# Optimization experiments

Hardware: AMD Instinct MI355X
Metric: run time of the kernel (lower is better)

## Reference

```python
import jax, jax.numpy as jnp
import numpy as np

NPOINT = 1024
RADIUS = 0.2
NSAMPLE = 32
FILTERS = [64, 64, 128]
BN_EPS = 1e-3  # Keras BatchNormalization default epsilon


def setup_inputs() -> dict:
    key = jax.random.key(0)
    ks = jax.random.split(key, 2 + 4 * len(FILTERS))
    xyz = jax.random.uniform(ks[0], (8, 4096, 3), dtype=jnp.float32)
    points = jax.random.normal(ks[1], (8, 4096, 64), dtype=jnp.float32)
    inp = {"xyz": xyz, "points": points}
    c_in = 64 + 3  # use_xyz concat
    for i, f in enumerate(FILTERS):
        k = 2 + 4 * i
        inp[f"w{i}"] = jax.random.normal(ks[k], (c_in, f), dtype=jnp.float32) * (1.0 / np.sqrt(c_in))
        inp[f"b{i}"] = jnp.zeros((f,), jnp.float32)
        inp[f"g{i}"] = 1.0 + 0.1 * jax.random.normal(ks[k + 2], (f,), dtype=jnp.float32)
        inp[f"be{i}"] = 0.1 * jax.random.normal(ks[k + 3], (f,), dtype=jnp.float32)
        c_in = f
    return inp


def farthest_point_sample(npoint, xyz):
    # xyz: (B, A, 3) -> idx (B, npoint), sequential FPS starting at point 0
    B, A, _ = xyz.shape
    def step(carry, _):
        dists, farthest = carry
        centroid = jnp.take_along_axis(xyz, farthest[:, None, None], axis=1)  # (B,1,3)
        d = jnp.sum((xyz - centroid) ** 2, axis=-1)                            # (B,A)
        dists = jnp.minimum(dists, d)
        nxt = jnp.argmax(dists, axis=-1).astype(jnp.int32)
        return (dists, nxt), farthest
    init = (jnp.full((B, A), 1e10, xyz.dtype), jnp.zeros((B,), jnp.int32))
    _, idx = jax.lax.scan(step, init, None, length=npoint)  # (npoint, B)
    return idx.T  # (B, npoint)


def query_ball_point(radius, nsample, xyz, new_xyz):
    # xyz: (B,A,3), new_xyz: (B,N,3) -> idx (B,N,nsample)
    A = xyz.shape[1]
    d2 = jnp.sum((new_xyz[:, :, None, :] - xyz[:, None, :, :]) ** 2, axis=-1)  # (B,N,A)
    mask = d2 < radius * radius
    cand = jnp.where(mask, jnp.arange(A, dtype=jnp.int32), jnp.int32(A))
    cand = jnp.sort(cand, axis=-1)[..., :nsample]           # first in-ball indices
    first = cand[..., :1]
    idx = jnp.where(cand == A, first, cand)                  # pad with first found
    idx = jnp.where(idx == A, 0, idx)                        # empty ball -> 0
    return idx


def group_point(points, idx):
    # points: (B,A,C), idx: (B,N,S) -> (B,N,S,C)
    return jax.vmap(lambda p, i: p[i])(points, idx)


def _forward(xyz, points, params):
    fps_idx = jax.lax.stop_gradient(farthest_point_sample(NPOINT, xyz))
    new_xyz = jnp.take_along_axis(xyz, fps_idx[:, :, None], axis=1)          # (B,N,3)
    idx = query_ball_point(RADIUS, NSAMPLE, jax.lax.stop_gradient(xyz),
                           jax.lax.stop_gradient(new_xyz))
    grouped_xyz = group_point(xyz, idx) - new_xyz[:, :, None, :]             # (B,N,S,3)
    grouped = jnp.concatenate([group_point(points, idx), grouped_xyz], -1)   # (B,N,S,C+3)
    h = grouped
    for (w, b, g, be) in params:
        h = jnp.einsum('bnsc,cf->bnsf', h, w) + b    # shared 1x1 conv
        h = g * h / jnp.sqrt(1.0 + BN_EPS) + be      # inference BN (mean=0, var=1)
        h = jax.nn.relu(h)
    new_points = jnp.max(h, axis=2)                  # max-pool over nsample
    return new_xyz, new_points


def reference(xyz, points, w0, b0, g0, be0, w1, b1, g1, be1, w2, b2, g2, be2):
    params = [(w0, b0, g0, be0), (w1, b1, g1, be1), (w2, b2, g2, be2)]
    return _forward(xyz, points, params)
```

## Files before the change

kernel.cpp:

```cpp
#include <hip/hip_runtime.h>

#define NPTS 4096
#define NQ   1024
#define NB   8
#define XTW  36

#define FPS_T  512
#define FPS_W  8
#define PPT    8
#define FPS_NB 8
#define WRK_NB 240
#define NWRK   (WRK_NB * 8)
#define WSLICE 10496
#define SMEM_BYTES (WSLICE * 8)

template <int CTRL, int RM>
__device__ __forceinline__ int dppi(int v) {
  return __builtin_amdgcn_update_dpp(v, v, CTRL, RM, 0xf, false);
}

template <int CTRL, int RM>
__device__ __forceinline__ double dpp_keymax(double k) {
  long long i = __double_as_longlong(k);
  int lo = (int)(unsigned)((unsigned long long)i & 0xffffffffull);
  int hi = (int)(unsigned)((unsigned long long)i >> 32);
  int plo = dppi<CTRL, RM>(lo);
  int phi = dppi<CTRL, RM>(hi);
  double o = __longlong_as_double(
      (long long)(((unsigned long long)(unsigned)phi << 32) | (unsigned)plo));
  return fmax(k, o);
}

__device__ __forceinline__ double wave_keymax(double k) {
  k = dpp_keymax<0x111, 0xf>(k);
  k = dpp_keymax<0x112, 0xf>(k);
  k = dpp_keymax<0x114, 0xf>(k);
  k = dpp_keymax<0x118, 0xf>(k);
  k = dpp_keymax<0x142, 0xa>(k);
  k = dpp_keymax<0x143, 0xc>(k);
  return k;
}

template <int C>
__device__ __forceinline__ float dppq(float v) {
  return __int_as_float(__builtin_amdgcn_update_dpp(
      __float_as_int(v), __float_as_int(v), C, 0xf, 0xf, false));
}

__device__ void fps_role(const float* __restrict__ xyz,
                         float* __restrict__ out_newxyz,
                         int* __restrict__ ws_idx, char* smem)
{
  const int b    = blockIdx.x;
  const int t    = threadIdx.x;
  const int lane = t & 63;
  const int wave = t >> 6;

  float* sxyz4 = (float*)smem;
  double (*swk)[FPS_W] = (double(*)[FPS_W])(smem + NPTS * 16);

  const float* xb = xyz + (size_t)b * NPTS * 3;
  for (int p = t; p < NPTS; p += FPS_T) {
    sxyz4[p * 4 + 0] = xb[p * 3 + 0];
    sxyz4[p * 4 + 1] = xb[p * 3 + 1];
    sxyz4[p * 4 + 2] = xb[p * 3 + 2];
    sxyz4[p * 4 + 3] = 0.0f;
  }
  __syncthreads();

  float px[PPT], py[PPT], pz[PPT], dst[PPT];
  unsigned ilo[PPT];
#pragma unroll
  for (int k = 0; k < PPT; ++k) {
    int p = t + (k << 9);
    px[k] = sxyz4[p * 4 + 0];
    py[k] = sxyz4[p * 4 + 1];
    pz[k] = sxyz4[p * 4 + 2];
    dst[k] = 1e10f;
    ilo[k] = ~(unsigned)p;
  }

  int farh0 = 0, farh1 = 0;
  int far = 0;
  for (int n = 0; n < NQ; ++n) {
    const float4 c = *(const float4*)(sxyz4 + far * 4);
    if (t == 0)
      __hip_atomic_store(ws_idx + (b << 10) + n, far,
                         __ATOMIC_RELAXED, __HIP_MEMORY_SCOPE_AGENT);
    if ((n & (FPS_T - 1)) == t) {
      if (n >> 9) farh1 = far; else farh0 = far;
    }

    double kk[PPT];
#pragma unroll
    for (int k = 0; k < PPT; ++k) {
      float dx = __fsub_rn(px[k], c.x);
      float dy = __fsub_rn(py[k], c.y);
      float dz = __fsub_rn(pz[k], c.z);
      float d2 = __fadd_rn(__fadd_rn(__fmul_rn(dx, dx), __fmul_rn(dy, dy)),
                           __fmul_rn(dz, dz));
      float dm = fminf(dst[k], d2);
      dst[k] = dm;
      kk[k] = __longlong_as_double((long long)(
          ((unsigned long long)__float_as_uint(dm) << 32) | ilo[k]));
    }
    double m0 = fmax(kk[0], kk[1]);
    double m1 = fmax(kk[2], kk[3]);
    double m2 = fmax(kk[4], kk[5]);
    double m3 = fmax(kk[6], kk[7]);
    double best = fmax(fmax(m0, m1), fmax(m2, m3));
    best = wave_keymax(best);

    long long bi = __double_as_longlong(best);
    unsigned blo = (unsigned)__builtin_amdgcn_readlane(
        (int)(unsigned)((unsigned long long)bi & 0xffffffffull), 63);
    unsigned bhi = (unsigned)__builtin_amdgcn_readlane(
        (int)(unsigned)((unsigned long long)bi >> 32), 63);
    double wkey = __longlong_as_double(
        (long long)(((unsigned long long)bhi << 32) | blo));

    const int par = n & 1;
    if (lane == 0) swk[par][wave] = wkey;
    __syncthreads();

    const double2* sp = (const double2*)swk[par];
    double2 a0 = sp[0], a1 = sp[1], a2 = sp[2], a3 = sp[3];
    double mk = fmax(fmax(fmax(a0.x, a0.y), fmax(a1.x, a1.y)),
                     fmax(fmax(a2.x, a2.y), fmax(a3.x, a3.y)));
    far = (int)(~(unsigned)((unsigned long long)__double_as_longlong(mk)));
  }

  {
    float4 c0 = *(const float4*)(sxyz4 + farh0 * 4);
    float* o0 = out_newxyz + ((size_t)b * NQ + t) * 3;
    o0[0] = c0.x; o0[1] = c0.y; o0[2] = c0.z;
    float4 c1 = *(const float4*)(sxyz4 + farh1 * 4);
    float* o1 = out_newxyz + ((size_t)b * NQ + FPS_T + t) * 3;
    o1[0] = c1.x; o1[1] = c1.y; o1[2] = c1.z;
  }
}

__device__ __forceinline__ void mlp_acc(float* __restrict__ acc,
                                        const float* __restrict__ XTb,
                                        const float* __restrict__ wg,
                                        int ldw, int nk, int fg, int sg)
{
#pragma unroll
  for (int i = 0; i < 32; ++i) acc[i] = 0.0f;
  const float* xrow = XTb + sg * 4;
  const float* wrow = wg + fg * 8;
#pragma unroll 4
  for (int k = 0; k < nk; ++k) {
    const float4 x  = *(const float4*)(xrow + k * XTW);
    const float4 wa = *(const float4*)(wrow + (size_t)k * ldw);
    const float4 wb = *(const float4*)(wrow + (size_t)k * ldw + 4);
    acc[0]  = fmaf(wa.x, x.x, acc[0]);  acc[1]  = fmaf(wa.x, x.y, acc[1]);
    acc[2]  = fmaf(wa.x, x.z, acc[2]);  acc[3]  = fmaf(wa.x, x.w, acc[3]);
    acc[4]  = fmaf(wa.y, x.x, acc[4]);  acc[5]  = fmaf(wa.y, x.y, acc[5]);
    acc[6]  = fmaf(wa.y, x.z, acc[6]);  acc[7]  = fmaf(wa.y, x.w, acc[7]);
    acc[8]  = fmaf(wa.z, x.x, acc[8]);  acc[9]  = fmaf(wa.z, x.y, acc[9]);
    acc[10] = fmaf(wa.z, x.z, acc[10]); acc[11] = fmaf(wa.z, x.w, acc[11]);
    acc[12] = fmaf(wa.w, x.x, acc[12]); acc[13] = fmaf(wa.w, x.y, acc[13]);
    acc[14] = fmaf(wa.w, x.z, acc[14]); acc[15] = fmaf(wa.w, x.w, acc[15]);
    acc[16] = fmaf(wb.x, x.x, acc[16]); acc[17] = fmaf(wb.x, x.y, acc[17]);
    acc[18] = fmaf(wb.x, x.z, acc[18]); acc[19] = fmaf(wb.x, x.w, acc[19]);
    acc[20] = fmaf(wb.y, x.x, acc[20]); acc[21] = fmaf(wb.y, x.y, acc[21]);
    acc[22] = fmaf(wb.y, x.z, acc[22]); acc[23] = fmaf(wb.y, x.w, acc[23]);
    acc[24] = fmaf(wb.z, x.x, acc[24]); acc[25] = fmaf(wb.z, x.y, acc[25]);
    acc[26] = fmaf(wb.z, x.z, acc[26]); acc[27] = fmaf(wb.z, x.w, acc[27]);
    acc[28] = fmaf(wb.w, x.x, acc[28]); acc[29] = fmaf(wb.w, x.y, acc[29]);
    acc[30] = fmaf(wb.w, x.z, acc[30]); acc[31] = fmaf(wb.w, x.w, acc[31]);
  }
}

__device__ __forceinline__ void store_layer(const float* __restrict__ acc,
                                            float* __restrict__ XTb,
                                            const float* __restrict__ g,
                                            const float* __restrict__ bi,
                                            const float* __restrict__ be,
                                            int fg, int sg, float RSQ)
{
  const float4 ga = *(const float4*)(g  + fg * 8);
  const float4 gb = *(const float4*)(g  + fg * 8 + 4);
  const float4 ba = *(const float4*)(bi + fg * 8);
  const float4 bb = *(const float4*)(bi + fg * 8 + 4);
  const float4 ea = *(const float4*)(be + fg * 8);
  const float4 eb = *(const float4*)(be + fg * 8 + 4);
  float sv[8] = {ga.x * RSQ, ga.y * RSQ, ga.z * RSQ, ga.w * RSQ,
                 gb.x * RSQ, gb.y * RSQ, gb.z * RSQ, gb.w * RSQ};
  float bv[8] = {ba.x, ba.y, ba.z, ba.w, bb.x, bb.y, bb.z, bb.w};
  float ev[8] = {ea.x, ea.y, ea.z, ea.w, eb.x, eb.y, eb.z, eb.w};
#pragma unroll
  for (int j = 0; j < 8; ++j) {
    float tv = fmaf(bv[j], sv[j], ev[j]);
    float4 h;
    h.x = fmaxf(fmaf(acc[j * 4 + 0], sv[j], tv), 0.0f);
    h.y = fmaxf(fmaf(acc[j * 4 + 1], sv[j], tv), 0.0f);
    h.z = fmaxf(fmaf(acc[j * 4 + 2], sv[j], tv), 0.0f);
    h.w = fmaxf(fmaf(acc[j * 4 + 3], sv[j], tv), 0.0f);
    *(float4*)(XTb + (fg * 8 + j) * XTW + sg * 4) = h;
  }
}

__device__ void worker_query(int q, int idx,
    const float* __restrict__ xyz, const float* __restrict__ pts,
    const float* __restrict__ w0, const float* __restrict__ b0,
    const float* __restrict__ g0, const float* __restrict__ be0,
    const float* __restrict__ w1, const float* __restrict__ b1,
    const float* __restrict__ g1, const float* __restrict__ be1,
    const float* __restrict__ w2, const float* __restrict__ b2,
    const float* __restrict__ g2, const float* __restrict__ be2,
    float* __restrict__ outp, float* __restrict__ XT, int* __restrict__ bidx,
    int lane)
{
  const int b = q >> 10;
  const float* xb = xyz + (size_t)b * NPTS * 3;
  const float cx = xb[idx * 3 + 0];
  const float cy = xb[idx * 3 + 1];
  const float cz = xb[idx * 3 + 2];

  int cnt = 0;
  float x0 = xb[lane * 3 + 0], y0 = xb[lane * 3 + 1], z0 = xb[lane * 3 + 2];
  float x1 = xb[(64 + lane) * 3 + 0], y1 = xb[(64 + lane) * 3 + 1],
        z1 = xb[(64 + lane) * 3 + 2];
  for (int ch = 0; ch < 64; ++ch) {
    const int an = (min(ch + 2, 63) << 6) | lane;
    float nx = xb[an * 3 + 0], ny = xb[an * 3 + 1], nz = xb[an * 3 + 2];
    float dx = __fsub_rn(cx, x0);
    float dy = __fsub_rn(cy, y0);
    float dz = __fsub_rn(cz, z0);
    float d2 = __fadd_rn(__fadd_rn(__fmul_rn(dx, dx), __fmul_rn(dy, dy)),
                         __fmul_rn(dz, dz));
    bool in = d2 < 0.04f;
    unsigned long long bal = __ballot(in);
    int pos = cnt + (int)__popcll(bal & ((1ull << lane) - 1ull));
    if (in && pos < 32) bidx[pos] = (ch << 6) | lane;
    cnt += (int)__popcll(bal);
    x0 = x1; y0 = y1; z0 = z1;
    x1 = nx; y1 = ny; z1 = nz;
    if (cnt >= 32) break;
  }
  if (cnt > 32) cnt = 32;
  int i0 = bidx[0];
  if (lane < 32 && lane >= cnt) bidx[lane] = i0;
  __builtin_amdgcn_wave_barrier();

  const int s  = lane & 31;
  const int kc = lane >> 5;
  const int is = bidx[s];
  const float4* pr4 = (const float4*)(pts + ((size_t)(b * NPTS + is)) * 64 + kc * 32);
  float* xcol = XT + s;
#pragma unroll
  for (int c = 0; c < 8; ++c) {
    float4 v = pr4[c];
    xcol[(kc * 32 + c * 4 + 0) * XTW] = v.x;
    xcol[(kc * 32 + c * 4 + 1) * XTW] = v.y;
    xcol[(kc * 32 + c * 4 + 2) * XTW] = v.z;
    xcol[(kc * 32 + c * 4 + 3) * XTW] = v.w;
  }
  if (kc == 0) {
    float ax = xb[is * 3 + 0], ay = xb[is * 3 + 1], az = xb[is * 3 + 2];
    xcol[64 * XTW] = ax - cx;
    xcol[65 * XTW] = ay - cy;
    xcol[66 * XTW] = az - cz;
  }
  __builtin_amdgcn_wave_barrier();

  const int fg = lane >> 3;
  const int sg = lane & 7;
  const float RSQ = rsqrtf(1.0f + 0.001f);
  float acc[32];

  mlp_acc(acc, XT, w0, 64, 67, fg, sg);
  store_layer(acc, XT, g0, b0, be0, fg, sg, RSQ);
  __builtin_amdgcn_wave_barrier();

  mlp_acc(acc, XT, w1, 64, 64, fg, sg);
  store_layer(acc, XT, g1, b1, be1, fg, sg, RSQ);
  __builtin_amdgcn_wave_barrier();

#pragma unroll
  for (int pass = 0; pass < 2; ++pass) {
    const int fofs = pass << 6;
    mlp_acc(acc, XT, w2 + fofs, 128, 64, fg, sg);
    const float4 ga = *(const float4*)(g2  + fofs + fg * 8);
    const float4 gb = *(const float4*)(g2  + fofs + fg * 8 + 4);
    const float4 ba = *(const float4*)(b2  + fofs + fg * 8);
    const float4 bb = *(const float4*)(b2  + fofs + fg * 8 + 4);
    const float4 ea = *(const float4*)(be2 + fofs + fg * 8);
    const float4 eb = *(const float4*)(be2 + fofs + fg * 8 + 4);
    float sv[8] = {ga.x * RSQ, ga.y * RSQ, ga.z * RSQ, ga.w * RSQ,
                   gb.x * RSQ, gb.y * RSQ, gb.z * RSQ, gb.w * RSQ};
    float bv[8] = {ba.x, ba.y, ba.z, ba.w, bb.x, bb.y, bb.z, bb.w};
    float ev[8] = {ea.x, ea.y, ea.z, ea.w, eb.x, eb.y, eb.z, eb.w};
    float r[8];
#pragma unroll
    for (int j = 0; j < 8; ++j) {
      float mx = fmaxf(fmaxf(acc[j * 4 + 0], acc[j * 4 + 1]),
                       fmaxf(acc[j * 4 + 2], acc[j * 4 + 3]));
      float mn = fminf(fminf(acc[j * 4 + 0], acc[j * 4 + 1]),
                       fminf(acc[j * 4 + 2], acc[j * 4 + 3]));
      mx = fmaxf(mx, dppq<0xB1>(mx));
      mx = fmaxf(mx, dppq<0x4E>(mx));
      mx = fmaxf(mx, dppq<0x141>(mx));
      mn = fminf(mn, dppq<0xB1>(mn));
      mn = fminf(mn, dppq<0x4E>(mn));
      mn = fminf(mn, dppq<0x141>(mn));
      float tv = fmaf(bv[j], sv[j], ev[j]);
      float m  = (sv[j] >= 0.0f) ? mx : mn;
      r[j] = fmaxf(fmaf(sv[j], m, tv), 0.0f);
    }
    if (sg == 0) {
      float* o = outp + (size_t)q * 128 + fofs + fg * 8;
      *(float4*)(o)     = make_float4(r[0], r[1], r[2], r[3]);
      *(float4*)(o + 4) = make_float4(r[4], r[5], r[6], r[7]);
    }
  }
}

__global__ __launch_bounds__(FPS_T, 1) void fused_kernel(
    const float* __restrict__ xyz, const float* __restrict__ pts,
    const float* __restrict__ w0, const float* __restrict__ b0,
    const float* __restrict__ g0, const float* __restrict__ be0,
    const float* __restrict__ w1, const float* __restrict__ b1,
    const float* __restrict__ g1, const float* __restrict__ be1,
    const float* __restrict__ w2, const float* __restrict__ b2,
    const float* __restrict__ g2, const float* __restrict__ be2,
    float* __restrict__ newxyz, float* __restrict__ newpts,
    int* __restrict__ ws_idx)
{
  __shared__ __align__(16) char smem[SMEM_BYTES];

  if (blockIdx.x < FPS_NB) {
    fps_role(xyz, newxyz, ws_idx, smem);
    return;
  }

  const int lane = threadIdx.x & 63;
  const int wave = threadIdx.x >> 6;
  char* sl = smem + wave * WSLICE;
  float* XT  = (float*)sl;
  int* bidx  = (int*)(sl + 9648);

  const int W = (blockIdx.x - FPS_NB) * 8 + wave;
  for (int g = W; g < NB * NQ; g += NWRK) {
    const int b = g & 7;
    const int n = g >> 3;
    const int q = (b << 10) | n;

    const int* slot = ws_idx + q;
    int idx = __hip_atomic_load(slot, __ATOMIC_RELAXED, __HIP_MEMORY_SCOPE_AGENT);
    int spins = 0;
    while ((unsigned)idx >= (unsigned)NPTS) {
      __builtin_amdgcn_s_sleep(16);
      idx = __hip_atomic_load(slot, __ATOMIC_RELAXED, __HIP_MEMORY_SCOPE_AGENT);
      if (++spins > 32768) { idx &= (NPTS - 1); break; }
    }

    worker_query(q, idx, xyz, pts, w0, b0, g0, be0, w1, b1, g1, be1,
                 w2, b2, g2, be2, newpts, XT, bidx, lane);
  }
}

extern "C" void kernel_launch(void* const* d_in, const int* in_sizes, int n_in,
                              void* d_out, int out_size, void* d_ws, size_t ws_size,
                              hipStream_t stream)
{
  const float* xyz = (const float*)d_in[0];
  const float* pts = (const float*)d_in[1];
  const float* w0  = (const float*)d_in[2];
  const float* b0  = (const float*)d_in[3];
  const float* g0  = (const float*)d_in[4];
  const float* be0 = (const float*)d_in[5];
  const float* w1  = (const float*)d_in[6];
  const float* b1  = (const float*)d_in[7];
  const float* g1  = (const float*)d_in[8];
  const float* be1 = (const float*)d_in[9];
  const float* w2  = (const float*)d_in[10];
  const float* b2  = (const float*)d_in[11];
  const float* g2  = (const float*)d_in[12];
  const float* be2 = (const float*)d_in[13];

  float* out    = (float*)d_out;
  float* newxyz = out;
  float* newpts = out + NB * NQ * 3;
  int*   ws_idx = (int*)d_ws;

  hipMemsetAsync(d_ws, 0xAA, (size_t)NB * NQ * sizeof(int), stream);

  hipLaunchKernelGGL(fused_kernel, dim3(FPS_NB + WRK_NB), dim3(FPS_T), 0, stream,
                     xyz, pts, w0, b0, g0, be0, w1, b1, g1, be1,
                     w2, b2, g2, be2, newxyz, newpts, ws_idx);
}
```

Measured before the change: 666.6 us.

## Restructure FPS to four waves with float max and ballot argmax

The farthest-point-sampling role now uses only 4 of its 8 waves, each thread holding 16 points, so the per-iteration block reduction combines fewer partials. The packed 64-bit key max reduction is replaced by a float max reduction across the wave, followed by a ballot pass to recover the lowest matching index. Sampled indices are also batched and published 8 at a time instead of one store per iteration. The aim is to shorten the serial per-iteration latency of FPS, at the cost of more work per thread and extra ballot instructions.

```diff
diff --git a/kernel.cpp b/kernel.cpp
--- a/kernel.cpp
+++ b/kernel.cpp
@@ -6,8 +6,8 @@
 #define XTW  36
 
 #define FPS_T  512
-#define FPS_W  8
-#define PPT    8
+#define FPW    4
+#define SLOTS  16
 #define FPS_NB 8
 #define WRK_NB 240
 #define NWRK   (WRK_NB * 8)
@@ -15,30 +15,19 @@
 #define SMEM_BYTES (WSLICE * 8)
 
 template <int CTRL, int RM>
-__device__ __forceinline__ int dppi(int v) {
-  return __builtin_amdgcn_update_dpp(v, v, CTRL, RM, 0xf, false);
-}
-
-template <int CTRL, int RM>
-__device__ __forceinline__ double dpp_keymax(double k) {
-  long long i = __double_as_longlong(k);
-  int lo = (int)(unsigned)((unsigned long long)i & 0xffffffffull);
-  int hi = (int)(unsigned)((unsigned long long)i >> 32);
-  int plo = dppi<CTRL, RM>(lo);
-  int phi = dppi<CTRL, RM>(hi);
-  double o = __longlong_as_double(
-      (long long)(((unsigned long long)(unsigned)phi << 32) | (unsigned)plo));
-  return fmax(k, o);
-}
-
-__device__ __forceinline__ double wave_keymax(double k) {
-  k = dpp_keymax<0x111, 0xf>(k);
-  k = dpp_keymax<0x112, 0xf>(k);
-  k = dpp_keymax<0x114, 0xf>(k);
-  k = dpp_keymax<0x118, 0xf>(k);
-  k = dpp_keymax<0x142, 0xa>(k);
-  k = dpp_keymax<0x143, 0xc>(k);
-  return k;
+__device__ __forceinline__ float dppf(float v) {
+  return __int_as_float(__builtin_amdgcn_update_dpp(
+      __float_as_int(v), __float_as_int(v), CTRL, RM, 0xf, false));
+}
+
+__device__ __forceinline__ float wave_max_f(float v) {
+  v = fmaxf(v, dppf<0x111, 0xf>(v));
+  v = fmaxf(v, dppf<0x112, 0xf>(v));
+  v = fmaxf(v, dppf<0x114, 0xf>(v));
+  v = fmaxf(v, dppf<0x118, 0xf>(v));
+  v = fmaxf(v, dppf<0x142, 0xa>(v));
+  v = fmaxf(v, dppf<0x143, 0xc>(v));
+  return v;
 }
 
 template <int C>
@@ -57,7 +46,7 @@
   const int wave = t >> 6;
 
   float* sxyz4 = (float*)smem;
-  double (*swk)[FPS_W] = (double(*)[FPS_W])(smem + NPTS * 16);
+  double (*swk)[FPW] = (double(*)[FPW])(smem + NPTS * 16);
 
   const float* xb = xyz + (size_t)b * NPTS * 3;
   for (int p = t; p < NPTS; p += FPS_T) {
@@ -68,75 +57,81 @@
   }
   __syncthreads();
 
-  float px[PPT], py[PPT], pz[PPT], dst[PPT];
-  unsigned ilo[PPT];
-#pragma unroll
-  for (int k = 0; k < PPT; ++k) {
-    int p = t + (k << 9);
-    px[k] = sxyz4[p * 4 + 0];
-    py[k] = sxyz4[p * 4 + 1];
-    pz[k] = sxyz4[p * 4 + 2];
-    dst[k] = 1e10f;
-    ilo[k] = ~(unsigned)p;
-  }
-
-  int farh0 = 0, farh1 = 0;
+  float px[SLOTS], py[SLOTS], pz[SLOTS], dst[SLOTS];
+  if (wave < FPW) {
+#pragma unroll
+    for (int k = 0; k < SLOTS; ++k) {
+      int p = t + (k << 8);
+      px[k] = sxyz4[p * 4 + 0];
+      py[k] = sxyz4[p * 4 + 1];
+      pz[k] = sxyz4[p * 4 + 2];
+      dst[k] = 1e10f;
+    }
+  }
+
   int far = 0;
+  int fkeep = 0;
+  int farh[4] = {0, 0, 0, 0};
+
   for (int n = 0; n < NQ; ++n) {
-    const float4 c = *(const float4*)(sxyz4 + far * 4);
-    if (t == 0)
-      __hip_atomic_store(ws_idx + (b << 10) + n, far,
-                         __ATOMIC_RELAXED, __HIP_MEMORY_SCOPE_AGENT);
-    if ((n & (FPS_T - 1)) == t) {
-      if (n >> 9) farh1 = far; else farh0 = far;
-    }
-
-    double kk[PPT];
-#pragma unroll
-    for (int k = 0; k < PPT; ++k) {
-      float dx = __fsub_rn(px[k], c.x);
-      float dy = __fsub_rn(py[k], c.y);
-      float dz = __fsub_rn(pz[k], c.z);
-      float d2 = __fadd_rn(__fadd_rn(__fmul_rn(dx, dx), __fmul_rn(dy, dy)),
-                           __fmul_rn(dz, dz));
-      float dm = fminf(dst[k], d2);
-      dst[k] = dm;
-      kk[k] = __longlong_as_double((long long)(
-          ((unsigned long long)__float_as_uint(dm) << 32) | ilo[k]));
-    }
-    double m0 = fmax(kk[0], kk[1]);
-    double m1 = fmax(kk[2], kk[3]);
-    double m2 = fmax(kk[4], kk[5]);
-    double m3 = fmax(kk[6], kk[7]);
-    double best = fmax(fmax(m0, m1), fmax(m2, m3));
-    best = wave_keymax(best);
-
-    long long bi = __double_as_longlong(best);
-    unsigned blo = (unsigned)__builtin_amdgcn_readlane(
-        (int)(unsigned)((unsigned long long)bi & 0xffffffffull), 63);
-    unsigned bhi = (unsigned)__builtin_amdgcn_readlane(
-        (int)(unsigned)((unsigned long long)bi >> 32), 63);
-    double wkey = __longlong_as_double(
-        (long long)(((unsigned long long)bhi << 32) | blo));
-
-    const int par = n & 1;
-    if (lane == 0) swk[par][wave] = wkey;
+    if (wave < FPW) {
+      const float4 c = *(const float4*)(sxyz4 + far * 4);
+      if (wave == 0 && lane == (n & 7)) fkeep = far;
+      if ((n & 255) == t) farh[n >> 8] = far;
+
+#pragma unroll
+      for (int k = 0; k < SLOTS; ++k) {
+        float dx = __fsub_rn(px[k], c.x);
+        float dy = __fsub_rn(py[k], c.y);
+        float dz = __fsub_rn(pz[k], c.z);
+        float d2 = __fadd_rn(__fadd_rn(__fmul_rn(dx, dx), __fmul_rn(dy, dy)),
+                             __fmul_rn(dz, dz));
+        dst[k] = fminf(dst[k], d2);
+      }
+      float m0 = fmaxf(fmaxf(dst[0],  dst[1]),  dst[2]);
+      float m1 = fmaxf(fmaxf(dst[3],  dst[4]),  dst[5]);
+      float m2 = fmaxf(fmaxf(dst[6],  dst[7]),  dst[8]);
+      float m3 = fmaxf(fmaxf(dst[9],  dst[10]), dst[11]);
+      float m4 = fmaxf(fmaxf(dst[12], dst[13]), dst[14]);
+      float ma = fmaxf(fmaxf(m0, m1), m2);
+      float mb = fmaxf(fmaxf(m3, m4), dst[15]);
+      float m  = fmaxf(ma, mb);
+      m = wave_max_f(m);
+      const float ms = __int_as_float(
+          __builtin_amdgcn_readlane(__float_as_int(m), 63));
+
+      int idxw = 0;
+#pragma unroll
+      for (int k = SLOTS - 1; k >= 0; --k) {
+        unsigned long long mask = __ballot(dst[k] == ms);
+        if (mask) idxw = (k << 8) + (wave << 6) + (int)__builtin_ctzll(mask);
+      }
+      if (lane == 0) {
+        unsigned long long kb =
+            ((unsigned long long)__float_as_uint(ms) << 32) |
+            (unsigned)(~(unsigned)idxw);
+        swk[n & 1][wave] = __longlong_as_double((long long)kb);
+      }
+    }
     __syncthreads();
-
-    const double2* sp = (const double2*)swk[par];
-    double2 a0 = sp[0], a1 = sp[1], a2 = sp[2], a3 = sp[3];
-    double mk = fmax(fmax(fmax(a0.x, a0.y), fmax(a1.x, a1.y)),
-                     fmax(fmax(a2.x, a2.y), fmax(a3.x, a3.y)));
-    far = (int)(~(unsigned)((unsigned long long)__double_as_longlong(mk)));
-  }
-
-  {
-    float4 c0 = *(const float4*)(sxyz4 + farh0 * 4);
-    float* o0 = out_newxyz + ((size_t)b * NQ + t) * 3;
-    o0[0] = c0.x; o0[1] = c0.y; o0[2] = c0.z;
-    float4 c1 = *(const float4*)(sxyz4 + farh1 * 4);
-    float* o1 = out_newxyz + ((size_t)b * NQ + FPS_T + t) * 3;
-    o1[0] = c1.x; o1[1] = c1.y; o1[2] = c1.z;
+    if (wave < FPW) {
+      const double2* sp = (const double2*)swk[n & 1];
+      double2 a0 = sp[0], a1 = sp[1];
+      double mk = fmax(fmax(a0.x, a0.y), fmax(a1.x, a1.y));
+      far = (int)(~(unsigned)((unsigned long long)__double_as_longlong(mk)));
+      if (wave == 0 && lane < 8 && (n & 7) == 7)
+        __hip_atomic_store(ws_idx + (b << 10) + (n & ~7) + lane, fkeep,
+                           __ATOMIC_RELAXED, __HIP_MEMORY_SCOPE_AGENT);
+    }
+  }
+
+  if (wave < FPW) {
+#pragma unroll
+    for (int j = 0; j < 4; ++j) {
+      float4 c = *(const float4*)(sxyz4 + farh[j] * 4);
+      float* o = out_newxyz + ((size_t)b * NQ + (j << 8) + t) * 3;
+      o[0] = c.x; o[1] = c.y; o[2] = c.z;
+    }
   }
 }
 
```

Result: slower. 801.9 us (+20.3%).
